# Kernel optimization log

Hardware: AMD Instinct MI355X
Metric: run time of the kernel (lower is better)

The kernel has to match this reference:

```python
import jax, jax.numpy as jnp
import numpy as np

FS = 16000.0
SOUND_SPEED = 343.0
MAX_ORDER = 10
FILTER_LEN = 81            # fractional-delay sinc filter taps (torchaudio default)
PAD = FILTER_LEN // 2      # 40
RIR_LEN = 8000             # static RIR length; bounds max delay for 10 m rooms, order 10

# ---- static image-source lattice: all (i,j,k) with |i|+|j|+|k| <= MAX_ORDER ----
_ind = np.arange(-MAX_ORDER, MAX_ORDER + 1)
_g = np.stack(np.meshgrid(_ind, _ind, _ind, indexing="ij"), -1).reshape(-1, 3)
_g = _g[np.abs(_g).sum(-1) <= MAX_ORDER]                      # (n_img=1561, 3)
XYZ = jnp.asarray(_g, dtype=jnp.float32)                      # (n_img, 3)
EXP_LO = jnp.asarray(np.abs(np.floor(_g / 2.0)), jnp.float32)        # reflections off x=0/y=0/z=0 walls
EXP_HI = jnp.asarray(np.abs(np.floor((_g + 1) / 2.0)), jnp.float32)  # reflections off far walls
ODD = jnp.asarray(_g % 2 == 1)                                # (n_img, 3) bool


def _hann(x, T):
    # truncated Hann window used by the fractional-delay filter
    return jnp.where(jnp.abs(x) <= T / 2, 0.5 * (1.0 + jnp.cos(2.0 * jnp.pi * x / T)), 0.0)


def _rir_one(room, mic, src, absorption):
    # room, mic, src: (3,) metres; absorption: (6,) per-wall absorption coeff
    # image-source positions: mirror source across walls per parity of lattice index
    img = jnp.where(ODD, room * (XYZ + 1.0) - src, room * XYZ + src)   # (n_img, 3)
    tr = jnp.sqrt(1.0 - absorption)                                     # wall reflection coeffs (6,)
    att = jnp.prod((tr[::2] ** EXP_LO) * (tr[1::2] ** EXP_HI), axis=-1)  # (n_img,)
    dist = jnp.linalg.norm(img - mic, axis=-1)                           # (n_img,)
    amp = att / dist                                                     # 1/r spreading
    delay = dist * FS / SOUND_SPEED                                      # delay in samples (float)
    delay_i = jnp.ceil(delay)                                            # integer anchor
    n = jnp.arange(-PAD, PAD + 1, dtype=jnp.float32)                     # (81,)
    x = n[None, :] + delay_i[:, None] - delay[:, None]                   # (n_img, 81)
    irs = amp[:, None] * jnp.sinc(x) * _hann(x, 2 * PAD)                 # windowed-sinc frac delay
    # scatter-add each 81-tap filter at offset delay_i - PAD into the RIR buffer
    idx = delay_i.astype(jnp.int32)[:, None] - PAD + jnp.arange(FILTER_LEN, dtype=jnp.int32)
    valid = (idx >= 0) & (idx < RIR_LEN)
    rir = jnp.zeros((RIR_LEN,), irs.dtype).at[jnp.clip(idx, 0, RIR_LEN - 1)].add(
        jnp.where(valid, irs, 0.0))
    return rir


def setup_inputs() -> dict:
    key = jax.random.key(0)
    k1, k2, k3, k4 = jax.random.split(key, 4)
    B = 256
    room = 3.0 + 7.0 * jax.random.uniform(k1, (B, 3), jnp.float32)       # room dims in [3,10] m
    mic_f = 0.05 + 0.40 * jax.random.uniform(k2, (B, 3), jnp.float32)    # mic frac in [0.05,0.45]
    src_f = 0.55 + 0.40 * jax.random.uniform(k3, (B, 3), jnp.float32)    # src frac in [0.55,0.95]
    absorp = 0.1 + 0.4 * jax.random.uniform(k4, (B, 1), jnp.float32)     # absorption in [0.1,0.5]
    inp = jnp.concatenate([room, mic_f, src_f, absorp], axis=1)          # (B, 10)
    return {"input": inp}


def reference(input):
    room = input[:, 0:3]
    mic = input[:, 3:6] * room
    src = input[:, 6:9] * room
    absorption = jnp.repeat(input[:, 9:10], 6, axis=1)                   # uniform over 6 walls
    rir = jax.vmap(_rir_one)(room, mic, src, absorption)                 # (B, RIR_LEN)
    dist = jnp.linalg.norm(mic - src, axis=1)
    toa = 40.0 + FS * dist / SOUND_SPEED                                 # (B,)
    return rir, toa
```

## Files before the change

kernel.cpp:

```cpp
#include <hip/hip_runtime.h>
#include <math.h>

#define NB 256
#define NIMG 1561
#define RIRLEN 8000
#define PADI 40
#define NTHREADS 1024
#define NWAVES (NTHREADS / 64)
#define NBKT 505
#define NSTARTP 512
#define NPAIR 63

struct ImgTab { unsigned int v[NIMG]; };

constexpr ImgTab build_tab() {
    ImgTab t{};
    int n = 0;
    for (int x = -10; x <= 10; ++x)
        for (int y = -10; y <= 10; ++y)
            for (int z = -10; z <= 10; ++z) {
                int ax = x < 0 ? -x : x;
                int ay = y < 0 ? -y : y;
                int az = z < 0 ? -z : z;
                int l1 = ax + ay + az;
                if (l1 <= 10) {
                    t.v[n++] = (unsigned)(x + 10) | ((unsigned)(y + 10) << 5) |
                               ((unsigned)(z + 10) << 10) | ((unsigned)l1 << 15);
                }
            }
    return t;
}

constexpr int tab_count() {
    int n = 0;
    for (int x = -10; x <= 10; ++x)
        for (int y = -10; y <= 10; ++y)
            for (int z = -10; z <= 10; ++z) {
                int ax = x < 0 ? -x : x;
                int ay = y < 0 ? -y : y;
                int az = z < 0 ? -z : z;
                if (ax + ay + az <= 10) ++n;
            }
    return n;
}
static_assert(tab_count() == NIMG, "image count mismatch");

__constant__ ImgTab c_tab = build_tab();

__global__ __launch_bounds__(NTHREADS) void
rir_kernel(const float* __restrict__ in, float* __restrict__ out) {
    __shared__ float4 s_rec[NIMG + 1];
    __shared__ float  s_trpow[11];
    __shared__ int    s_hist[NSTARTP];
    __shared__ int    s_start[NSTARTP];
    __shared__ int    s_cursor[NBKT];
    __shared__ int    s_qnext;
    __shared__ int    s_nspike;
    __shared__ int    s_spike_idx[64];
    __shared__ float  s_spike_amp[64];

    const int b   = blockIdx.x;
    const int tid = threadIdx.x;
    const float* p = in + b * 10;

    if (tid < NSTARTP) s_hist[tid] = 0;
    if (tid == 0) {
        float tr = sqrtf(1.0f - p[9]);
        float pw = 1.0f;
        for (int k = 0; k <= 10; ++k) { s_trpow[k] = pw; pw *= tr; }
        s_nspike = 0;
        s_qnext  = NWAVES;
        s_rec[NIMG] = make_float4(0.0f, 0.0f, 0.0f, -1.0e6f);
    }
    __syncthreads();

    const float rx = p[0], ry = p[1], rz = p[2];
    const float mx = p[3] * rx, my = p[4] * ry, mz = p[5] * rz;
    const float sx = p[6] * rx, sy = p[7] * ry, sz = p[8] * rz;
    const float K = 16000.0f / 343.0f;
    const float INV_PI = 0.31830988618379067154f;

    float4 rec[2];
    int ibkt[2]  = {0, 0};
    bool ivalid[2] = {false, false};

    for (int u = 0; u < 2; ++u) {
        int i = tid + u * NTHREADS;
        if (i < NIMG) {
            unsigned v = c_tab.v[i];
            int gx = (int)(v & 31u) - 10;
            int gy = (int)((v >> 5) & 31u) - 10;
            int gz = (int)((v >> 10) & 31u) - 10;
            int l1 = (int)(v >> 15);

            float ix = (gx & 1) ? rx * (float)(gx + 1) - sx : rx * (float)gx + sx;
            float iy = (gy & 1) ? ry * (float)(gy + 1) - sy : ry * (float)gy + sy;
            float iz = (gz & 1) ? rz * (float)(gz + 1) - sz : rz * (float)gz + sz;

            float dx = ix - mx, dy = iy - my, dz = iz - mz;
            float dist = sqrtf(dx * dx + dy * dy + dz * dz);

            float amp  = s_trpow[l1] * __builtin_amdgcn_rcpf(dist);
            float d    = dist * K;
            float dlc  = ceilf(d);
            float frac = dlc - d;
            int   idlc = (int)dlc;
            int   base = idlc - PADI;

            if (base < RIRLEN) {
                if (frac == 0.0f) {
                    if (idlc < RIRLEN) {
                        int sp = atomicAdd(&s_nspike, 1);
                        if (sp < 64) { s_spike_idx[sp] = idlc; s_spike_amp[sp] = amp; }
                    }
                } else {
                    float spf = (frac < 1.0e-3f) ? frac : (sinpif(frac) * INV_PI);
                    float S   = amp * spf;
                    if (idlc & 1) S = -S;
                    float hS  = 0.5f * S;
                    float cd  = cospif(d * 0.025f);
                    float sd  = sinpif(d * 0.025f);
                    rec[u] = make_float4(hS, hS * cd, hS * sd, d);
                    ibkt[u]   = (base + 80) >> 4;
                    ivalid[u] = true;
                    atomicAdd(&s_hist[ibkt[u]], 1);
                }
            }
        }
    }
    __syncthreads();

    if (tid < 64) {
        int base_i = tid * 8;
        int v[8], pre[8];
        int run = 0;
#pragma unroll
        for (int j = 0; j < 8; ++j) {
            v[j] = s_hist[base_i + j];
            pre[j] = run;
            run += v[j];
        }
        int t = run;
#pragma unroll
        for (int d2 = 1; d2 < 64; d2 <<= 1) {
            int y = __shfl_up(t, d2);
            if (tid >= d2) t += y;
        }
        int excl = t - run;
#pragma unroll
        for (int j = 0; j < 8; ++j) {
            int idx = base_i + j;
            int sv  = excl + pre[j];
            s_start[idx] = sv;
            if (idx < NBKT) s_cursor[idx] = sv;
        }
    }
    __syncthreads();

    for (int u = 0; u < 2; ++u) {
        if (ivalid[u]) {
            int pos = atomicAdd(&s_cursor[ibkt[u]], 1);
            s_rec[pos] = rec[u];
        }
    }
    __syncthreads();

    const int wave = tid >> 6;
    const int lane = tid & 63;
    const int h    = lane >> 5;
    const int l5   = lane & 31;
    const float sgn = (l5 & 1) ? -1.0f : 1.0f;
    const float c32 = -0.80901699437494742410f;
    const float s32 =  0.58778525229247312917f;
    float* __restrict__ ob = out + (size_t)b * RIRLEN;

    int q = wave;
    while (q < NPAIR) {
        const int n0 = (q << 7) + (h << 6) + l5;
        const int n1 = n0 + 32;
        const float fn0 = (float)n0;
        const float cn0 = cospif(fn0 * 0.025f), sn0 = sinpif(fn0 * 0.025f);
        const float cnn1 = cn0 * c32 - sn0 * s32;
        const float snn1 = sn0 * c32 + cn0 * s32;

        const int loA = s_start[8 * q];
        const int hiA = s_start[8 * q + 9];
        const int loB = s_start[8 * q + 4];
        const int hiB = s_start[8 * q + 13];
        const int lenA = hiA - loA, lenB = hiB - loB;
        const int lmin = (lenA < lenB) ? lenA : lenB;
        const int lmax = (lenA > lenB) ? lenA : lenB;
        const int lo   = h ? loB : loA;
        const int hi   = h ? hiB : hiA;

        float acc0 = 0.0f, acc1 = 0.0f;
#pragma clang loop unroll_count(8)
        for (int it = 0; it < lmin; ++it) {
            float4 r = s_rec[lo + it];
            float x0 = fn0 - r.w;
            float x1 = x0 + 32.0f;
            float pr = __builtin_amdgcn_rcpf(x0 * x1);
            float t0 = fmaf(r.y, cn0, r.x);  t0 = fmaf(r.z, sn0, t0);
            float t1 = fmaf(r.y, cnn1, r.x); t1 = fmaf(r.z, snn1, t1);
            t0 = (fabsf(x0) < 40.0f) ? t0 : 0.0f;
            t1 = (fabsf(x1) < 40.0f) ? t1 : 0.0f;
            acc0 = fmaf(t0 * x1, pr, acc0);
            acc1 = fmaf(t1 * x0, pr, acc1);
        }
#pragma clang loop unroll_count(4)
        for (int it = lmin; it < lmax; ++it) {
            int k = lo + it;
            float4 r = s_rec[(k < hi) ? k : NIMG];
            float x0 = fn0 - r.w;
            float x1 = x0 + 32.0f;
            float pr = __builtin_amdgcn_rcpf(x0 * x1);
            float t0 = fmaf(r.y, cn0, r.x);  t0 = fmaf(r.z, sn0, t0);
            float t1 = fmaf(r.y, cnn1, r.x); t1 = fmaf(r.z, snn1, t1);
            t0 = (fabsf(x0) < 40.0f) ? t0 : 0.0f;
            t1 = (fabsf(x1) < 40.0f) ? t1 : 0.0f;
            acc0 = fmaf(t0 * x1, pr, acc0);
            acc1 = fmaf(t1 * x0, pr, acc1);
        }
        if (n0 < RIRLEN) ob[n0] = acc0 * sgn;
        if (n1 < RIRLEN) ob[n1] = acc1 * sgn;

        int nq;
        if (lane == 0) nq = atomicAdd(&s_qnext, 1);
        q = __shfl(nq, 0);
    }

    __syncthreads();
    int nsp = s_nspike; nsp = (nsp < 64) ? nsp : 64;
    if (tid < nsp) atomicAdd(&ob[s_spike_idx[tid]], s_spike_amp[tid]);

    if (tid == 0) {
        float dx = mx - sx, dy = my - sy, dz = mz - sz;
        out[(size_t)NB * RIRLEN + b] = 40.0f + sqrtf(dx * dx + dy * dy + dz * dz) * K;
    }
}

extern "C" void kernel_launch(void* const* d_in, const int* in_sizes, int n_in,
                              void* d_out, int out_size, void* d_ws, size_t ws_size,
                              hipStream_t stream) {
    const float* in = (const float*)d_in[0];
    float* out = (float*)d_out;
    rir_kernel<<<dim3(NB), dim3(NTHREADS), 0, stream>>>(in, out);
}
```

Measured before the change: 77.23 us.

## Split output tiles into fixed-size image chunks and accumulate in shared memory

Each 128-sample output tile was one work item whose loop length was its full bucket-range image count. Tiles are now split into chunks of 64 images, and a wave-level scan builds a work list ordered from the last tile to the first. Waves pull chunks dynamically, which is meant to spread uneven per-tile work more evenly across the 16 waves. Partial sums go into a shared-memory RIR buffer through LDS atomics, and spikes are added there too, before one vectorised float4 copy to global memory. In exchange it adds 32 KB of LDS, extra atomics, and repeated per-chunk setup trig.

```diff
diff --git a/kernel.cpp b/kernel.cpp
--- a/kernel.cpp
+++ b/kernel.cpp
@@ -10,6 +10,8 @@
 #define NBKT 505
 #define NSTARTP 512
 #define NPAIR 63
+#define CHUNK 64
+#define MAXITEMS 256
 
 struct ImgTab { unsigned int v[NIMG]; };
 
@@ -50,20 +52,25 @@
 __global__ __launch_bounds__(NTHREADS) void
 rir_kernel(const float* __restrict__ in, float* __restrict__ out) {
     __shared__ float4 s_rec[NIMG + 1];
+    __shared__ float  s_out[RIRLEN];
     __shared__ float  s_trpow[11];
     __shared__ int    s_hist[NSTARTP];
     __shared__ int    s_start[NSTARTP];
     __shared__ int    s_cursor[NBKT];
+    __shared__ int    s_T;
     __shared__ int    s_qnext;
     __shared__ int    s_nspike;
     __shared__ int    s_spike_idx[64];
     __shared__ float  s_spike_amp[64];
 
+    int* const s_item = s_hist;
+
     const int b   = blockIdx.x;
     const int tid = threadIdx.x;
     const float* p = in + b * 10;
 
     if (tid < NSTARTP) s_hist[tid] = 0;
+    for (int i = tid; i < RIRLEN; i += NTHREADS) s_out[i] = 0.0f;
     if (tid == 0) {
         float tr = sqrtf(1.0f - p[9]);
         float pw = 1.0f;
@@ -163,6 +170,27 @@
             s_rec[pos] = rec[u];
         }
     }
+
+    if (tid < 64) {
+        int nch = 0, q = 62 - tid;
+        if (tid < NPAIR) {
+            int lenA = s_start[8 * q + 9]  - s_start[8 * q];
+            int lenB = s_start[8 * q + 13] - s_start[8 * q + 4];
+            int ml   = (lenA > lenB) ? lenA : lenB;
+            nch = (ml + CHUNK - 1) >> 6;
+        }
+        int run = nch;
+#pragma unroll
+        for (int d2 = 1; d2 < 64; d2 <<= 1) {
+            int y = __shfl_up(run, d2);
+            if (tid >= d2) run += y;
+        }
+        int excl = run - nch;
+        int tot  = __shfl(run, 63);
+        if (tid == 0) s_T = (tot < MAXITEMS) ? tot : MAXITEMS;
+        for (int c = 0; c < nch; ++c)
+            if (excl + c < MAXITEMS) s_item[excl + c] = (q << 5) | c;
+    }
     __syncthreads();
 
     const int wave = tid >> 6;
@@ -173,9 +201,12 @@
     const float c32 = -0.80901699437494742410f;
     const float s32 =  0.58778525229247312917f;
     float* __restrict__ ob = out + (size_t)b * RIRLEN;
-
-    int q = wave;
-    while (q < NPAIR) {
+    const int T = s_T;
+
+    int idx = wave;
+    while (idx < T) {
+        const int item = s_item[idx];
+        const int q = item >> 5, c = item & 31;
         const int n0 = (q << 7) + (h << 6) + l5;
         const int n1 = n0 + 32;
         const float fn0 = (float)n0;
@@ -188,14 +219,17 @@
         const int loB = s_start[8 * q + 4];
         const int hiB = s_start[8 * q + 13];
         const int lenA = hiA - loA, lenB = hiB - loB;
-        const int lmin = (lenA < lenB) ? lenA : lenB;
-        const int lmax = (lenA > lenB) ? lenA : lenB;
-        const int lo   = h ? loB : loA;
-        const int hi   = h ? hiB : hiA;
+        const int lmn = (lenA < lenB) ? lenA : lenB;
+        const int lmx = (lenA > lenB) ? lenA : lenB;
+        const int st  = c << 6;
+        int e0 = lmn - st; e0 = (e0 < 0) ? 0 : ((e0 > CHUNK) ? CHUNK : e0);
+        int e1 = lmx - st; e1 = (e1 > CHUNK) ? CHUNK : e1;
+        const int lo = (h ? loB : loA) + st;
+        const int hi = h ? hiB : hiA;
 
         float acc0 = 0.0f, acc1 = 0.0f;
 #pragma clang loop unroll_count(8)
-        for (int it = 0; it < lmin; ++it) {
+        for (int it = 0; it < e0; ++it) {
             float4 r = s_rec[lo + it];
             float x0 = fn0 - r.w;
             float x1 = x0 + 32.0f;
@@ -208,7 +242,7 @@
             acc1 = fmaf(t1 * x0, pr, acc1);
         }
 #pragma clang loop unroll_count(4)
-        for (int it = lmin; it < lmax; ++it) {
+        for (int it = e0; it < e1; ++it) {
             int k = lo + it;
             float4 r = s_rec[(k < hi) ? k : NIMG];
             float x0 = fn0 - r.w;
@@ -221,17 +255,23 @@
             acc0 = fmaf(t0 * x1, pr, acc0);
             acc1 = fmaf(t1 * x0, pr, acc1);
         }
-        if (n0 < RIRLEN) ob[n0] = acc0 * sgn;
-        if (n1 < RIRLEN) ob[n1] = acc1 * sgn;
+        if (n0 < RIRLEN) atomicAdd(&s_out[n0], acc0 * sgn);
+        if (n1 < RIRLEN) atomicAdd(&s_out[n1], acc1 * sgn);
 
         int nq;
         if (lane == 0) nq = atomicAdd(&s_qnext, 1);
-        q = __shfl(nq, 0);
+        idx = __shfl(nq, 0);
     }
 
     __syncthreads();
     int nsp = s_nspike; nsp = (nsp < 64) ? nsp : 64;
-    if (tid < nsp) atomicAdd(&ob[s_spike_idx[tid]], s_spike_amp[tid]);
+    if (tid < nsp) atomicAdd(&s_out[s_spike_idx[tid]], s_spike_amp[tid]);
+    __syncthreads();
+
+    float4* __restrict__ o4 = (float4*)ob;
+    const float4* s4 = (const float4*)s_out;
+#pragma unroll 2
+    for (int i = tid; i < RIRLEN / 4; i += NTHREADS) o4[i] = s4[i];
 
     if (tid == 0) {
         float dx = mx - sx, dy = my - sy, dz = mz - sz;
```

New measurement: 79.35 us. +2.7%, slower.
